# Performance work log

Hardware: AMD Instinct MI355X
Metric: run time of the kernel (lower is better)

The kernel has to match this reference:

```python
import jax, jax.numpy as jnp
import numpy as np

B, S, F, H, L = 4096, 512, 8, 10, 2


def setup_inputs() -> dict:
    key = jax.random.key(0)
    ks = jax.random.split(key, 12)
    bound = 1.0 / np.sqrt(H)  # PyTorch LSTM/Linear init scale
    u = lambda k, shape: jax.random.uniform(k, shape, jnp.float32, -bound, bound)
    return {
        "input_tensor": jax.random.normal(ks[0], (B, S, F), jnp.float32),
        "hidden": jnp.zeros((L, B, H), jnp.float32),
        "cell": jnp.zeros((L, B, H), jnp.float32),
        # layer 0 (input size F), layer 1 (input size H); gate order i,f,g,o
        "W_ih0": u(ks[1], (4 * H, F)), "W_hh0": u(ks[2], (4 * H, H)),
        "b_ih0": u(ks[3], (4 * H,)),   "b_hh0": u(ks[4], (4 * H,)),
        "W_ih1": u(ks[5], (4 * H, H)), "W_hh1": u(ks[6], (4 * H, H)),
        "b_ih1": u(ks[7], (4 * H,)),   "b_hh1": u(ks[8], (4 * H,)),
        "W_fc": u(ks[9], (1, H)),      "b_fc": u(ks[10], (1,)),
    }


def _lstm_layer(x_sbf, h0, c0, W_ih, W_hh, b_ih, b_hh):
    # x_sbf: [S, B, Fin]; h0,c0: [B, H]. Returns hs [S,B,H], (hT, cT).
    b = b_ih + b_hh

    def step(carry, x):
        h, c = carry
        gates = x @ W_ih.T + h @ W_hh.T + b  # [B, 4H]
        i, f, g, o = jnp.split(gates, 4, axis=-1)
        c = jax.nn.sigmoid(f) * c + jax.nn.sigmoid(i) * jnp.tanh(g)
        h = jax.nn.sigmoid(o) * jnp.tanh(c)
        return (h, c), h

    (hT, cT), hs = jax.lax.scan(step, (h0, c0), x_sbf)
    return hs, hT, cT


def reference(input_tensor, hidden, cell,
              W_ih0, W_hh0, b_ih0, b_hh0,
              W_ih1, W_hh1, b_ih1, b_hh1,
              W_fc, b_fc):
    x = jnp.transpose(input_tensor, (1, 0, 2))  # [S, B, F]
    hs0, h0T, c0T = _lstm_layer(x, hidden[0], cell[0], W_ih0, W_hh0, b_ih0, b_hh0)
    hs1, h1T, c1T = _lstm_layer(hs0, hidden[1], cell[1], W_ih1, W_hh1, b_ih1, b_hh1)
    out = hs1[-1]                      # last timestep, [B, H]
    out_regression = out @ W_fc.T + b_fc  # [B, 1]
    hidden_out = jnp.stack([h0T, h1T])
    cell_out = jnp.stack([c0T, c1T])
    return out_regression, hidden_out, cell_out
```

## Files before the change

kernel.cpp:

```cpp
#include <hip/hip_runtime.h>


typedef __fp16 v2h __attribute__((ext_vector_type(2)));

#define L2E 1.4426950408889634f

__device__ __forceinline__ v2h pkh(float a, float b) {
    return __builtin_amdgcn_cvt_pkrtz(a, b);
}
__device__ __forceinline__ float bpermf(int baddr, float v) {
    int r = __builtin_amdgcn_ds_bpermute(baddr, __builtin_bit_cast(int, v));
    return __builtin_bit_cast(float, r);
}

#define SIGM(a)  __builtin_amdgcn_rcpf(1.0f + __builtin_amdgcn_exp2f(-(a)))
#define TANHP(a) fmaf(-2.0f, __builtin_amdgcn_rcpf(1.0f + __builtin_amdgcn_exp2f(a)), 1.0f)
#define DOT2(acc, w, v) (acc) = __builtin_amdgcn_fdot2((w), (v), (acc), false)

__global__ __launch_bounds__(256, 2)
void lstm2_r8(const float* __restrict__ x,
              const float* __restrict__ hid,
              const float* __restrict__ cel,
              const float* __restrict__ Wih0, const float* __restrict__ Whh0,
              const float* __restrict__ bih0, const float* __restrict__ bhh0,
              const float* __restrict__ Wih1, const float* __restrict__ Whh1,
              const float* __restrict__ bih1, const float* __restrict__ bhh1,
              const float* __restrict__ Wfc,  const float* __restrict__ bfc,
              float* __restrict__ out)
{
    __shared__ __fp16 h0buf[8][6][20];
    __shared__ __fp16 h1buf[6][20];
    __shared__ float  fcb[6][10];

    const int tid  = threadIdx.x;
    const int lane = tid & 63;
    const int wid  = tid >> 6;
    const int uwid = __builtin_amdgcn_readfirstlane(wid);
    int grp = lane / 20;
    int l20 = lane - grp * 20;
    if (lane >= 60) { grp = 2; l20 = 19; }
    const int  ju       = (l20 < 10) ? l20 : l20 - 10;
    const bool unitlane = (l20 < 10);
    const int  eIw = (wid & 1) * 3 + grp;
    const int  e   = blockIdx.x * 6 + eIw;
    const int  ec  = (e < 4095) ? e : 4095;
    const int  baddr = ((l20 < 10) ? (lane + 10) : lane) * 4;

    const float alpha2 = unitlane ? 2.0f : 1.0f;
    const float beta2  = unitlane ? -1.0f : 0.0f;
    const float scB    = unitlane ? 2.0f * L2E : L2E;
    const int   rA = l20, rB = 20 + l20;

    if (uwid < 2) {
        v2h wxA[4], wxB[4], whA[5], whB[5];
        #pragma unroll
        for (int k = 0; k < 4; ++k) {
            wxA[k] = pkh(Wih0[rA*8+2*k]*L2E, Wih0[rA*8+2*k+1]*L2E);
            wxB[k] = pkh(Wih0[rB*8+2*k]*scB, Wih0[rB*8+2*k+1]*scB);
        }
        #pragma unroll
        for (int k = 0; k < 5; ++k) {
            whA[k] = pkh(Whh0[rA*10+2*k]*L2E, Whh0[rA*10+2*k+1]*L2E);
            whB[k] = pkh(Whh0[rB*10+2*k]*scB, Whh0[rB*10+2*k+1]*scB);
        }
        const float bA = (bih0[rA] + bhh0[rA]) * L2E;
        const float bB = (bih0[rB] + bhh0[rB]) * scB;

        v2h hv[5];
        #pragma unroll
        for (int k = 0; k < 5; ++k) hv[k] = pkh(hid[ec*10+2*k], hid[ec*10+2*k+1]);
        float cc = cel[ec * 10 + ju];
        float hj = 0.0f;

        __fp16* const wbase = &h0buf[0][eIw][0];
        __fp16* const wlane = wbase + l20;

        const float4* __restrict__ xp = reinterpret_cast<const float4*>(x + (size_t)ec * 4096);
        float4 xb0[2], xb1[2], xb2[2], xb3[2];
        xb0[0]=xp[0]; xb0[1]=xp[1];  xb1[0]=xp[2]; xb1[1]=xp[3];
        xb2[0]=xp[4]; xb2[1]=xp[5];  xb3[0]=xp[6]; xb3[1]=xp[7];

#define L0STEP(XB, S, TN)                                                    \
        {                                                                    \
            v2h x0=pkh(XB[0].x,XB[0].y), x1=pkh(XB[0].z,XB[0].w);            \
            v2h x2=pkh(XB[1].x,XB[1].y), x3=pkh(XB[1].z,XB[1].w);            \
            { int tn=(TN)>511?511:(TN); XB[0]=xp[2*tn]; XB[1]=xp[2*tn+1]; }  \
            float aA = bA, aB = bB;                                          \
            DOT2(aA,wxA[0],x0); DOT2(aB,wxB[0],x0);                          \
            DOT2(aA,wxA[1],x1); DOT2(aB,wxB[1],x1);                          \
            DOT2(aA,wxA[2],x2); DOT2(aB,wxB[2],x2);                          \
            DOT2(aA,wxA[3],x3); DOT2(aB,wxB[3],x3);                          \
            DOT2(aA,whA[0],hv[0]); DOT2(aB,whB[0],hv[0]);                    \
            DOT2(aA,whA[1],hv[1]); DOT2(aB,whB[1],hv[1]);                    \
            DOT2(aA,whA[2],hv[2]); DOT2(aB,whB[2],hv[2]);                    \
            DOT2(aA,whA[3],hv[3]); DOT2(aB,whB[3],hv[3]);                    \
            DOT2(aA,whA[4],hv[4]); DOT2(aB,whB[4],hv[4]);                    \
            float r1 = SIGM(aA);                                             \
            float r2 = __builtin_amdgcn_rcpf(1.0f + __builtin_amdgcn_exp2f(-aB)); \
            float act2 = fmaf(alpha2, r2, beta2);                            \
            float ig = r1 * act2;                                            \
            float sf = bpermf(baddr, r1);                                    \
            float so = bpermf(baddr, act2);                                  \
            cc = fmaf(sf, cc, ig);                                           \
            hj = so * TANHP((2.0f*L2E) * cc);                                \
            wlane[(S)*120] = (__fp16)hj;                                     \
            { const v2h* rb = (const v2h*)(wbase + (S)*120);                 \
              hv[0]=rb[0]; hv[1]=rb[1]; hv[2]=rb[2]; hv[3]=rb[3]; hv[4]=rb[4]; } \
        }

        for (int it = 0; it < 64; ++it) {
            const int tb = 8 * it;
            L0STEP(xb0, 0, tb + 4)
            L0STEP(xb1, 1, tb + 5)
            L0STEP(xb2, 2, tb + 6)
            L0STEP(xb3, 3, tb + 7)
            __syncthreads();
            L0STEP(xb0, 4, tb + 8)
            L0STEP(xb1, 5, tb + 9)
            L0STEP(xb2, 6, tb + 10)
            L0STEP(xb3, 7, tb + 11)
            __syncthreads();
        }
#undef L0STEP

        __syncthreads();
        if (unitlane && e < 4096) {
            out[4096          + e * 10 + ju] = hj;
            out[4096 + 81920  + e * 10 + ju] = cc;
        }

    } else {
        v2h wiA[5], wiB[5], whA[5], whB[5];
        #pragma unroll
        for (int k = 0; k < 5; ++k) {
            wiA[k] = pkh(Wih1[rA*10+2*k]*L2E, Wih1[rA*10+2*k+1]*L2E);
            wiB[k] = pkh(Wih1[rB*10+2*k]*scB, Wih1[rB*10+2*k+1]*scB);
            whA[k] = pkh(Whh1[rA*10+2*k]*L2E, Whh1[rA*10+2*k+1]*L2E);
            whB[k] = pkh(Whh1[rB*10+2*k]*scB, Whh1[rB*10+2*k+1]*scB);
        }
        const float bA = (bih1[rA] + bhh1[rA]) * L2E;
        const float bB = (bih1[rB] + bhh1[rB]) * scB;
        const float wfc = Wfc[ju];

        v2h hv[5];
        #pragma unroll
        for (int k = 0; k < 5; ++k) hv[k] = pkh(hid[40960+ec*10+2*k], hid[40960+ec*10+2*k+1]);
        float cc = cel[40960 + ec * 10 + ju];
        float hj = 0.0f;

        const __fp16* const rbase = &h0buf[0][eIw][0];
        __fp16* const h1w  = &h1buf[eIw][0];
        __fp16* const h1wl = h1w + l20;

#define L1STEP(SR)                                                           \
        {                                                                    \
            const v2h* ir = (const v2h*)(rbase + (SR)*120);                  \
            v2h p0=ir[0], p1=ir[1], p2=ir[2], p3=ir[3], p4=ir[4];            \
            float aA = bA, aB = bB;                                          \
            DOT2(aA,wiA[0],p0); DOT2(aB,wiB[0],p0);                          \
            DOT2(aA,wiA[1],p1); DOT2(aB,wiB[1],p1);                          \
            DOT2(aA,wiA[2],p2); DOT2(aB,wiB[2],p2);                          \
            DOT2(aA,wiA[3],p3); DOT2(aB,wiB[3],p3);                          \
            DOT2(aA,wiA[4],p4); DOT2(aB,wiB[4],p4);                          \
            DOT2(aA,whA[0],hv[0]); DOT2(aB,whB[0],hv[0]);                    \
            DOT2(aA,whA[1],hv[1]); DOT2(aB,whB[1],hv[1]);                    \
            DOT2(aA,whA[2],hv[2]); DOT2(aB,whB[2],hv[2]);                    \
            DOT2(aA,whA[3],hv[3]); DOT2(aB,whB[3],hv[3]);                    \
            DOT2(aA,whA[4],hv[4]); DOT2(aB,whB[4],hv[4]);                    \
            float r1 = SIGM(aA);                                             \
            float r2 = __builtin_amdgcn_rcpf(1.0f + __builtin_amdgcn_exp2f(-aB)); \
            float act2 = fmaf(alpha2, r2, beta2);                            \
            float ig = r1 * act2;                                            \
            float sf = bpermf(baddr, r1);                                    \
            float so = bpermf(baddr, act2);                                  \
            cc = fmaf(sf, cc, ig);                                           \
            hj = so * TANHP((2.0f*L2E) * cc);                                \
            h1wl[0] = (__fp16)hj;                                            \
            { const v2h* rb = (const v2h*)h1w;                               \
              hv[0]=rb[0]; hv[1]=rb[1]; hv[2]=rb[2]; hv[3]=rb[3]; hv[4]=rb[4]; } \
        }

        for (int it = 0; it < 64; ++it) {
            __syncthreads();
            L1STEP(0)
            L1STEP(1)
            L1STEP(2)
            L1STEP(3)
            __syncthreads();
            L1STEP(4)
            L1STEP(5)
            L1STEP(6)
            L1STEP(7)
        }
#undef L1STEP

        if (unitlane) fcb[eIw][ju] = hj * wfc;
        __syncthreads();
        if (l20 == 0 && e < 4096) {
            float p = bfc[0];
            #pragma unroll
            for (int k = 0; k < 10; ++k) p += fcb[eIw][k];
            out[e] = p;
        }
        if (unitlane && e < 4096) {
            out[4096 + 40960  + e * 10 + ju] = hj;
            out[4096 + 122880 + e * 10 + ju] = cc;
        }
    }
}

extern "C" void kernel_launch(void* const* d_in, const int* in_sizes, int n_in,
                              void* d_out, int out_size, void* d_ws, size_t ws_size,
                              hipStream_t stream) {
    const float* x    = (const float*)d_in[0];
    const float* hid  = (const float*)d_in[1];
    const float* cel  = (const float*)d_in[2];
    const float* Wih0 = (const float*)d_in[3];
    const float* Whh0 = (const float*)d_in[4];
    const float* bih0 = (const float*)d_in[5];
    const float* bhh0 = (const float*)d_in[6];
    const float* Wih1 = (const float*)d_in[7];
    const float* Whh1 = (const float*)d_in[8];
    const float* bih1 = (const float*)d_in[9];
    const float* bhh1 = (const float*)d_in[10];
    const float* Wfc  = (const float*)d_in[11];
    const float* bfc  = (const float*)d_in[12];

    hipLaunchKernelGGL(lstm2_r8, dim3(683), dim3(256), 0, stream,
                       x, hid, cel, Wih0, Whh0, bih0, bhh0,
                       Wih1, Whh1, bih1, bhh1, Wfc, bfc,
                       (float*)d_out);
}
```

Baseline: 173.3 us.

## Software-pipeline input projections and double the layer handoff buffer depth

Both layers now compute the input-projection dot products for the next timestep ahead of the recurrent part of the current step, taking them off the serial h-dependency chain. The shared handoff buffer between the layers grows from 8 to 16 timesteps, so barriers occur half as often. Rows are padded to 24 halves and read with one 16-byte plus one 4-byte LDS load instead of five 4-byte loads. The cost is more live registers and more LDS, which could affect occupancy at the current launch bounds.

```diff
diff --git a/kernel.cpp b/kernel.cpp
--- a/kernel.cpp
+++ b/kernel.cpp
@@ -2,6 +2,8 @@
 
 
 typedef __fp16 v2h __attribute__((ext_vector_type(2)));
+typedef __fp16 v8h __attribute__((ext_vector_type(8)));
+struct h4 { v2h a, b, c, d; };
 
 #define L2E 1.4426950408889634f
 
@@ -18,19 +20,19 @@
 #define DOT2(acc, w, v) (acc) = __builtin_amdgcn_fdot2((w), (v), (acc), false)
 
 __global__ __launch_bounds__(256, 2)
-void lstm2_r8(const float* __restrict__ x,
-              const float* __restrict__ hid,
-              const float* __restrict__ cel,
-              const float* __restrict__ Wih0, const float* __restrict__ Whh0,
-              const float* __restrict__ bih0, const float* __restrict__ bhh0,
-              const float* __restrict__ Wih1, const float* __restrict__ Whh1,
-              const float* __restrict__ bih1, const float* __restrict__ bhh1,
-              const float* __restrict__ Wfc,  const float* __restrict__ bfc,
-              float* __restrict__ out)
+void lstm2_r10(const float* __restrict__ x,
+               const float* __restrict__ hid,
+               const float* __restrict__ cel,
+               const float* __restrict__ Wih0, const float* __restrict__ Whh0,
+               const float* __restrict__ bih0, const float* __restrict__ bhh0,
+               const float* __restrict__ Wih1, const float* __restrict__ Whh1,
+               const float* __restrict__ bih1, const float* __restrict__ bhh1,
+               const float* __restrict__ Wfc,  const float* __restrict__ bfc,
+               float* __restrict__ out)
 {
-    __shared__ __fp16 h0buf[8][6][20];
-    __shared__ __fp16 h1buf[6][20];
-    __shared__ float  fcb[6][10];
+    __shared__ __attribute__((aligned(16))) __fp16 h0buf[16][6][24];
+    __shared__ __attribute__((aligned(16))) __fp16 h1buf[6][24];
+    __shared__ float fcb[6][10];
 
     const int tid  = threadIdx.x;
     const int lane = tid & 63;
@@ -51,6 +53,12 @@
     const float scB    = unitlane ? 2.0f * L2E : L2E;
     const int   rA = l20, rB = 20 + l20;
 
+#define READROW(PTR, H)                                                      \
+    { v8h w0_ = *(const v8h*)(PTR);                                          \
+      v2h w1_ = *(const v2h*)((PTR) + 8);                                    \
+      h4 q_ = __builtin_bit_cast(h4, w0_);                                   \
+      H[0]=q_.a; H[1]=q_.b; H[2]=q_.c; H[3]=q_.d; H[4]=w1_; }
+
     if (uwid < 2) {
         v2h wxA[4], wxB[4], whA[5], whB[5];
         #pragma unroll
@@ -80,16 +88,31 @@
         xb0[0]=xp[0]; xb0[1]=xp[1];  xb1[0]=xp[2]; xb1[1]=xp[3];
         xb2[0]=xp[4]; xb2[1]=xp[5];  xb3[0]=xp[6]; xb3[1]=xp[7];
 
-#define L0STEP(XB, S, TN)                                                    \
+        float axA[2], axB[2];
+        {
+            v2h x0=pkh(xb0[0].x,xb0[0].y), x1=pkh(xb0[0].z,xb0[0].w);
+            v2h x2=pkh(xb0[1].x,xb0[1].y), x3=pkh(xb0[1].z,xb0[1].w);
+            xb0[0]=xp[8]; xb0[1]=xp[9];
+            float nA=bA, nB=bB;
+            DOT2(nA,wxA[0],x0); DOT2(nB,wxB[0],x0);
+            DOT2(nA,wxA[1],x1); DOT2(nB,wxB[1],x1);
+            DOT2(nA,wxA[2],x2); DOT2(nB,wxB[2],x2);
+            DOT2(nA,wxA[3],x3); DOT2(nB,wxB[3],x3);
+            axA[0]=nA; axB[0]=nB;
+        }
+
+#define L0STEP(S, XB, TN, PC, PN)                                            \
         {                                                                    \
             v2h x0=pkh(XB[0].x,XB[0].y), x1=pkh(XB[0].z,XB[0].w);            \
             v2h x2=pkh(XB[1].x,XB[1].y), x3=pkh(XB[1].z,XB[1].w);            \
             { int tn=(TN)>511?511:(TN); XB[0]=xp[2*tn]; XB[1]=xp[2*tn+1]; }  \
-            float aA = bA, aB = bB;                                          \
-            DOT2(aA,wxA[0],x0); DOT2(aB,wxB[0],x0);                          \
-            DOT2(aA,wxA[1],x1); DOT2(aB,wxB[1],x1);                          \
-            DOT2(aA,wxA[2],x2); DOT2(aB,wxB[2],x2);                          \
-            DOT2(aA,wxA[3],x3); DOT2(aB,wxB[3],x3);                          \
+            float nA=bA, nB=bB;                                              \
+            DOT2(nA,wxA[0],x0); DOT2(nB,wxB[0],x0);                          \
+            DOT2(nA,wxA[1],x1); DOT2(nB,wxB[1],x1);                          \
+            DOT2(nA,wxA[2],x2); DOT2(nB,wxB[2],x2);                          \
+            DOT2(nA,wxA[3],x3); DOT2(nB,wxB[3],x3);                          \
+            axA[PN]=nA; axB[PN]=nB;                                          \
+            float aA=axA[PC], aB=axB[PC];                                    \
             DOT2(aA,whA[0],hv[0]); DOT2(aB,whB[0],hv[0]);                    \
             DOT2(aA,whA[1],hv[1]); DOT2(aB,whB[1],hv[1]);                    \
             DOT2(aA,whA[2],hv[2]); DOT2(aB,whB[2],hv[2]);                    \
@@ -103,22 +126,29 @@
             float so = bpermf(baddr, act2);                                  \
             cc = fmaf(sf, cc, ig);                                           \
             hj = so * TANHP((2.0f*L2E) * cc);                                \
-            wlane[(S)*120] = (__fp16)hj;                                     \
-            { const v2h* rb = (const v2h*)(wbase + (S)*120);                 \
-              hv[0]=rb[0]; hv[1]=rb[1]; hv[2]=rb[2]; hv[3]=rb[3]; hv[4]=rb[4]; } \
-        }
-
-        for (int it = 0; it < 64; ++it) {
-            const int tb = 8 * it;
-            L0STEP(xb0, 0, tb + 4)
-            L0STEP(xb1, 1, tb + 5)
-            L0STEP(xb2, 2, tb + 6)
-            L0STEP(xb3, 3, tb + 7)
-            __syncthreads();
-            L0STEP(xb0, 4, tb + 8)
-            L0STEP(xb1, 5, tb + 9)
-            L0STEP(xb2, 6, tb + 10)
-            L0STEP(xb3, 7, tb + 11)
+            wlane[(S)*144] = (__fp16)hj;                                     \
+            READROW(wbase + (S)*144, hv)                                     \
+        }
+
+        for (int it = 0; it < 32; ++it) {
+            const int tb = 16 * it;
+            L0STEP(0,  xb1, tb+5,  0, 1)
+            L0STEP(1,  xb2, tb+6,  1, 0)
+            L0STEP(2,  xb3, tb+7,  0, 1)
+            L0STEP(3,  xb0, tb+8,  1, 0)
+            L0STEP(4,  xb1, tb+9,  0, 1)
+            L0STEP(5,  xb2, tb+10, 1, 0)
+            L0STEP(6,  xb3, tb+11, 0, 1)
+            L0STEP(7,  xb0, tb+12, 1, 0)
+            __syncthreads();
+            L0STEP(8,  xb1, tb+13, 0, 1)
+            L0STEP(9,  xb2, tb+14, 1, 0)
+            L0STEP(10, xb3, tb+15, 0, 1)
+            L0STEP(11, xb0, tb+16, 1, 0)
+            L0STEP(12, xb1, tb+17, 0, 1)
+            L0STEP(13, xb2, tb+18, 1, 0)
+            L0STEP(14, xb3, tb+19, 0, 1)
+            L0STEP(15, xb0, tb+20, 1, 0)
             __syncthreads();
         }
 #undef L0STEP
@@ -152,16 +182,24 @@
         __fp16* const h1w  = &h1buf[eIw][0];
         __fp16* const h1wl = h1w + l20;
 
-#define L1STEP(SR)                                                           \
+        float axA[2], axB[2];
+
+#define L1PRE(S, P)                                                          \
         {                                                                    \
-            const v2h* ir = (const v2h*)(rbase + (SR)*120);                  \
-            v2h p0=ir[0], p1=ir[1], p2=ir[2], p3=ir[3], p4=ir[4];            \
-            float aA = bA, aB = bB;                                          \
-            DOT2(aA,wiA[0],p0); DOT2(aB,wiB[0],p0);                          \
-            DOT2(aA,wiA[1],p1); DOT2(aB,wiB[1],p1);                          \
-            DOT2(aA,wiA[2],p2); DOT2(aB,wiB[2],p2);                          \
-            DOT2(aA,wiA[3],p3); DOT2(aB,wiB[3],p3);                          \
-            DOT2(aA,wiA[4],p4); DOT2(aB,wiB[4],p4);                          \
+            v2h pr[5];                                                       \
+            READROW(rbase + (S)*144, pr)                                     \
+            float nA=bA, nB=bB;                                              \
+            DOT2(nA,wiA[0],pr[0]); DOT2(nB,wiB[0],pr[0]);                    \
+            DOT2(nA,wiA[1],pr[1]); DOT2(nB,wiB[1],pr[1]);                    \
+            DOT2(nA,wiA[2],pr[2]); DOT2(nB,wiB[2],pr[2]);                    \
+            DOT2(nA,wiA[3],pr[3]); DOT2(nB,wiB[3],pr[3]);                    \
+            DOT2(nA,wiA[4],pr[4]); DOT2(nB,wiB[4],pr[4]);                    \
+            axA[P]=nA; axB[P]=nB;                                            \
+        }
+
+#define L1CORE(PC)                                                           \
+        {                                                                    \
+            float aA=axA[PC], aB=axB[PC];                                    \
             DOT2(aA,whA[0],hv[0]); DOT2(aB,whB[0],hv[0]);                    \
             DOT2(aA,whA[1],hv[1]); DOT2(aB,whB[1],hv[1]);                    \
             DOT2(aA,whA[2],hv[2]); DOT2(aB,whB[2],hv[2]);                    \
@@ -176,23 +214,33 @@
             cc = fmaf(sf, cc, ig);                                           \
             hj = so * TANHP((2.0f*L2E) * cc);                                \
             h1wl[0] = (__fp16)hj;                                            \
-            { const v2h* rb = (const v2h*)h1w;                               \
-              hv[0]=rb[0]; hv[1]=rb[1]; hv[2]=rb[2]; hv[3]=rb[3]; hv[4]=rb[4]; } \
-        }
-
-        for (int it = 0; it < 64; ++it) {
-            __syncthreads();
-            L1STEP(0)
-            L1STEP(1)
-            L1STEP(2)
-            L1STEP(3)
-            __syncthreads();
-            L1STEP(4)
-            L1STEP(5)
-            L1STEP(6)
-            L1STEP(7)
-        }
-#undef L1STEP
+            READROW(h1w, hv)                                                 \
+        }
+
+        for (int it = 0; it < 32; ++it) {
+            __syncthreads();
+            L1PRE(0, 0)
+            L1PRE(1, 1) L1CORE(0)
+            L1PRE(2, 0) L1CORE(1)
+            L1PRE(3, 1) L1CORE(0)
+            L1PRE(4, 0) L1CORE(1)
+            L1PRE(5, 1) L1CORE(0)
+            L1PRE(6, 0) L1CORE(1)
+            L1PRE(7, 1) L1CORE(0)
+            L1CORE(1)
+            __syncthreads();
+            L1PRE(8, 0)
+            L1PRE(9,  1) L1CORE(0)
+            L1PRE(10, 0) L1CORE(1)
+            L1PRE(11, 1) L1CORE(0)
+            L1PRE(12, 0) L1CORE(1)
+            L1PRE(13, 1) L1CORE(0)
+            L1PRE(14, 0) L1CORE(1)
+            L1PRE(15, 1) L1CORE(0)
+            L1CORE(1)
+        }
+#undef L1PRE
+#undef L1CORE
 
         if (unitlane) fcb[eIw][ju] = hj * wfc;
         __syncthreads();
@@ -226,7 +274,7 @@
     const float* Wfc  = (const float*)d_in[11];
     const float* bfc  = (const float*)d_in[12];
 
-    hipLaunchKernelGGL(lstm2_r8, dim3(683), dim3(256), 0, stream,
+    hipLaunchKernelGGL(lstm2_r10, dim3(683), dim3(256), 0, stream,
                        x, hid, cel, Wih0, Whh0, bih0, bhh0,
                        Wih1, Whh1, bih1, bhh1, Wfc, bfc,
                        (float*)d_out);
```

After: 160.5 us. -7.4%, faster.
